# Performance work log

Hardware: AMD Instinct MI355X
Metric: run time of the kernel (lower is better)

The kernel has to match this reference:

```python
import jax, jax.numpy as jnp
import numpy as np
from jax import lax

SIGMA = 1.0
ALPHA = 1.0
BETA = 1.0
TRUNCATE = 4.0  # scipy.ndimage default


def _gauss_kernel(sigma):
    radius = int(TRUNCATE * sigma + 0.5)  # scipy radius rule -> 4 for sigma=1
    x = np.arange(-radius, radius + 1, dtype=np.float64)
    k = np.exp(-0.5 * (x / sigma) ** 2)
    k = (k / k.sum()).astype(np.float32)
    return k

_KERNEL = _gauss_kernel(SIGMA)


def _blur_axis(img, k, axis):
    # scipy mode='reflect' == jnp.pad mode='symmetric' (edge repeated)
    r = len(k) // 2
    pad = [(0, 0)] * img.ndim
    pad[axis] = (r, r)
    xp = jnp.pad(img, pad, mode='symmetric')
    n = img.shape[axis]
    out = k[0] * lax.slice_in_dim(xp, 0, n, axis=axis)
    for i in range(1, len(k)):
        out = out + k[i] * lax.slice_in_dim(xp, i, i + n, axis=axis)
    return out


def gaussian_blur(img):
    # scalar sigma in scipy blurs along EVERY axis, including batch & channel
    k = jnp.asarray(_KERNEL, dtype=img.dtype)
    for ax in range(img.ndim):
        img = _blur_axis(img, k, ax)
    return img


def decompose(I):
    I_log = jnp.log(I + 1e-6)
    I_smooth = gaussian_blur(I_log)
    R = I_log - I_smooth
    L = I_log - R  # == I_smooth
    return jnp.exp(L), jnp.exp(R)


def setup_inputs() -> dict:
    key = jax.random.key(0)
    k1, k2 = jax.random.split(key)
    shape = (16, 3, 512, 512)
    I_enhanced = jax.random.uniform(k1, shape, dtype=jnp.float32)
    I_gt = jax.random.uniform(k2, shape, dtype=jnp.float32)
    return {"I_enhanced": I_enhanced, "I_gt": I_gt}


def reference(I_enhanced, I_gt):
    L_enh, R_enh = decompose(I_enhanced)
    L_gt, R_gt = decompose(I_gt)
    L_reflectance = jnp.mean((R_enh - R_gt) ** 2)
    L_illumination = jnp.mean((L_enh - L_gt) ** 2)
    return ALPHA * L_reflectance + BETA * L_illumination
```

## Files before the change

kernel.cpp:

```cpp
#include <hip/hip_runtime.h>
#include <hip/hip_fp16.h>
#include <cmath>

#define PLANE (512*512)
#define NPLANES 48
#define NEL (48*PLANE)

struct Taps { float k[9]; };
struct CMat { float w[3][3]; };


__global__ __launch_bounds__(64)
void k_blur_hw(const float* __restrict__ inE, const float* __restrict__ inG,
               ushort* __restrict__ ws, Taps tp)
{
    const int l    = threadIdx.x;
    const int w0   = (blockIdx.x & 1) * 256;
    const int r0   = (blockIdx.x >> 1) * 32;
    const int z    = blockIdx.y;

    const float* src = (z < NPLANES) ? (inE + z * PLANE)
                                     : (inG + (z - NPLANES) * PLANE);

    const int  col   = w0 + 4 * l;
    const bool is0   = (l == 0);
    const bool is63  = (l == 63);
    const bool ledge = (w0 == 0);
    const bool redge = (w0 + 256 == 512);
    const bool do_halo = (is0 && !ledge) || (is63 && !redge);
    const int  hoff  = is0 ? (w0 - 4) : (w0 + 256);
    const int  tile  = col >> 6;
    const int  inner = col & 63;

    float ring[10][4];

#define FOLD(r) ((r) < 0 ? (-1 - (r)) : ((r) > 511 ? (1023 - (r)) : (r)))

    float4 pown[3], phal[3];
    phal[0] = phal[1] = phal[2] = make_float4(1.f, 1.f, 1.f, 1.f);
#pragma unroll
    for (int s = 0; s < 3; ++s) {
        const float* rp = src + FOLD(r0 - 4 + s) * 512;
        pown[s] = *(const float4*)(rp + col);
        if (do_halo) phal[s] = *(const float4*)(rp + hoff);
    }

    for (int jb = 0; jb < 40; jb += 10) {
#pragma unroll
        for (int u = 0; u < 10; ++u) {
            const int j = jb + u;

            float4 own = pown[0], hal = phal[0];
            pown[0] = pown[1]; pown[1] = pown[2];
            phal[0] = phal[1]; phal[1] = phal[2];
            if (j + 3 < 40) {
                const float* rp = src + FOLD(r0 - 1 + j) * 512;
                pown[2] = *(const float4*)(rp + col);
                if (do_halo) phal[2] = *(const float4*)(rp + hoff);
            }

            const float w4 = __logf(own.x + 1e-6f);
            const float w5 = __logf(own.y + 1e-6f);
            const float w6 = __logf(own.z + 1e-6f);
            const float w7 = __logf(own.w + 1e-6f);
            const float h0 = __logf(hal.x + 1e-6f);
            const float h1 = __logf(hal.y + 1e-6f);
            const float h2 = __logf(hal.z + 1e-6f);
            const float h3 = __logf(hal.w + 1e-6f);

            float win[12];
            win[4] = w4; win[5] = w5; win[6] = w6; win[7] = w7;
            win[0] = __shfl_up(w4, 1);
            win[1] = __shfl_up(w5, 1);
            win[2] = __shfl_up(w6, 1);
            win[3] = __shfl_up(w7, 1);
            win[8]  = __shfl_down(w4, 1);
            win[9]  = __shfl_down(w5, 1);
            win[10] = __shfl_down(w6, 1);
            win[11] = __shfl_down(w7, 1);
            if (is0) {
                if (ledge) { win[0] = w7; win[1] = w6; win[2] = w5; win[3] = w4; }
                else       { win[0] = h0; win[1] = h1; win[2] = h2; win[3] = h3; }
            }
            if (is63) {
                if (redge) { win[8] = w7; win[9] = w6; win[10] = w5; win[11] = w4; }
                else       { win[8] = h0; win[9] = h1; win[10] = h2; win[11] = h3; }
            }

#pragma unroll
            for (int i = 0; i < 4; ++i) {
                float o = 0.f;
#pragma unroll
                for (int t = 0; t < 9; ++t) o += tp.k[t] * win[i + t];
                ring[u][i] = o;
            }

            if (j >= 8) {
                float acc[4];
#pragma unroll
                for (int i = 0; i < 4; ++i) {
                    float o = 0.f;
#pragma unroll
                    for (int t = 0; t < 9; ++t)
                        o += tp.k[t] * ring[(u + 2 + t) % 10][i];
                    acc[i] = o;
                }
                const int ro = r0 + j - 8;
                __half2 pa, pb;
                pa.x = __float2half(acc[0]); pa.y = __float2half(acc[1]);
                pb.x = __float2half(acc[2]); pb.y = __float2half(acc[3]);
                ushort* dp = ws + (((ro * 8 + tile) * 96) + z) * 64 + inner;
                *(uint2*)dp = make_uint2(*(uint*)&pa, *(uint*)&pb);
            }
        }
    }
#undef FOLD
}

__global__ __launch_bounds__(256)
void k_cn_loss(const ushort* __restrict__ ws, const float* __restrict__ Ie,
               const float* __restrict__ Ig, float* __restrict__ out,
               Taps tp, CMat cm)
{
    const int tid = threadIdx.x;
    const int P   = blockIdx.x * 256 + tid;
    const int hw0 = P * 2;
    const ushort* wbase = ws + (hw0 >> 6) * (96 * 64) + (hw0 & 63);

    __half2 k2[9], cw[3][3];
#pragma unroll
    for (int t = 0; t < 9; ++t) k2[t] = __float2half2_rn(tp.k[t]);
#pragma unroll
    for (int i = 0; i < 3; ++i)
#pragma unroll
        for (int j = 0; j < 3; ++j) cw[i][j] = __float2half2_rn(cm.w[i][j]);

    __half2 re[9][3];
    __half2 rg[9][3];

#define LOADRAW(m, uE, uG)                                                     \
    uE[0] = *(const uint*)(wbase + ((m) * 3 + 0) * 64);                        \
    uE[1] = *(const uint*)(wbase + ((m) * 3 + 1) * 64);                        \
    uE[2] = *(const uint*)(wbase + ((m) * 3 + 2) * 64);                        \
    uG[0] = *(const uint*)(wbase + (48 + (m) * 3 + 0) * 64);                   \
    uG[1] = *(const uint*)(wbase + (48 + (m) * 3 + 1) * 64);                   \
    uG[2] = *(const uint*)(wbase + (48 + (m) * 3 + 2) * 64);

#define CBLUR(u, dst)                                                          \
    {                                                                          \
        __half2 v0 = *(__half2*)&u[0];                                         \
        __half2 v1 = *(__half2*)&u[1];                                         \
        __half2 v2 = *(__half2*)&u[2];                                         \
        dst[0] = __hfma2(cw[0][0], v0, __hfma2(cw[0][1], v1, __hmul2(cw[0][2], v2))); \
        dst[1] = __hfma2(cw[1][0], v0, __hfma2(cw[1][1], v1, __hmul2(cw[1][2], v2))); \
        dst[2] = __hfma2(cw[2][0], v0, __hfma2(cw[2][1], v1, __hmul2(cw[2][2], v2))); \
    }

#pragma unroll
    for (int m = 0; m < 4; ++m) {
        uint uE[3], uG[3];
        LOADRAW(m, uE, uG);
        CBLUR(uE, re[m]); CBLUR(uG, rg[m]);
    }
    uint nuE[3], nuG[3];
    LOADRAW(4, nuE, nuG);
    float2 ieq[3], igq[3];
#pragma unroll
    for (int c = 0; c < 3; ++c) {
        ieq[c] = *(const float2*)(Ie + c * PLANE + hw0);
        igq[c] = *(const float2*)(Ig + c * PLANE + hw0);
    }

    float acc = 0.f;
#pragma unroll
    for (int n = 0; n < 16; ++n) {
        float2 nie[3], nig[3];
        if (n + 1 < 16) {
#pragma unroll
            for (int c = 0; c < 3; ++c) {
                nie[c] = *(const float2*)(Ie + ((n + 1) * 3 + c) * PLANE + hw0);
                nig[c] = *(const float2*)(Ig + ((n + 1) * 3 + c) * PLANE + hw0);
            }
        }
        const int mnew = n + 4;
        if (mnew < 16) {
            CBLUR(nuE, re[mnew % 9]); CBLUR(nuG, rg[mnew % 9]);
            if (mnew + 1 < 16) { LOADRAW(mnew + 1, nuE, nuG); }
        }
#pragma unroll
        for (int c = 0; c < 3; ++c) {
            __half2 se2 = __float2half2_rn(0.f), sg2 = se2;
#pragma unroll
            for (int t = 0; t < 9; ++t) {
                int m = n - 4 + t;
                m = (m < 0) ? (-1 - m) : ((m > 15) ? (31 - m) : m);
                se2 = __hfma2(k2[t], re[m % 9][c], se2);
                sg2 = __hfma2(k2[t], rg[m % 9][c], sg2);
            }
            const float se0 = __half2float(__low2half(se2));
            const float se1 = __half2float(__high2half(se2));
            const float sg0 = __half2float(__low2half(sg2));
            const float sg1 = __half2float(__high2half(sg2));

            {
                float ee = __expf(-se0), eg = __expf(-sg0);
                float Re = (ieq[c].x + 1e-6f) * ee;
                float Rg = (igq[c].x + 1e-6f) * eg;
                float Le = __builtin_amdgcn_rcpf(ee);
                float Lg = __builtin_amdgcn_rcpf(eg);
                float dr = Re - Rg, dl = Le - Lg;
                acc += dr * dr + dl * dl;
            }
            {
                float ee = __expf(-se1), eg = __expf(-sg1);
                float Re = (ieq[c].y + 1e-6f) * ee;
                float Rg = (igq[c].y + 1e-6f) * eg;
                float Le = __builtin_amdgcn_rcpf(ee);
                float Lg = __builtin_amdgcn_rcpf(eg);
                float dr = Re - Rg, dl = Le - Lg;
                acc += dr * dr + dl * dl;
            }
        }
        if (n + 1 < 16) {
#pragma unroll
            for (int c = 0; c < 3; ++c) { ieq[c] = nie[c]; igq[c] = nig[c]; }
        }
    }
#undef LOADRAW
#undef CBLUR

    __shared__ float red[256];
    red[tid] = acc;
    __syncthreads();
#pragma unroll
    for (int s = 128; s > 0; s >>= 1) {
        if (tid < s) red[tid] += red[tid + s];
        __syncthreads();
    }
    if (tid == 0) atomicAdd(out, red[0] * (1.0f / (float)NEL));
}

extern "C" void kernel_launch(void* const* d_in, const int* in_sizes, int n_in,
                              void* d_out, int out_size, void* d_ws, size_t ws_size,
                              hipStream_t stream) {
    const float* Ie = (const float*)d_in[0];
    const float* Ig = (const float*)d_in[1];

    Taps tp;
    {
        double kk[9], s = 0.0;
        for (int i = 0; i < 9; ++i) { double x = (double)(i - 4); kk[i] = exp(-0.5 * x * x); s += kk[i]; }
        for (int i = 0; i < 9; ++i) tp.k[i] = (float)(kk[i] / s);
    }

    CMat cm;
    {
        for (int c = 0; c < 3; ++c) {
            cm.w[c][0] = cm.w[c][1] = cm.w[c][2] = 0.f;
            for (int t = 0; t < 9; ++t) {
                int m = c - 4 + t;
                int mm = ((m % 6) + 6) % 6;
                if (mm > 2) mm = 5 - mm;
                cm.w[c][mm] += tp.k[t];
            }
        }
    }

    ushort* ws = (ushort*)d_ws;

    hipMemsetAsync(d_out, 0, sizeof(float), stream);
    dim3 g1(32, 96);
    k_blur_hw<<<g1, 64, 0, stream>>>(Ie, Ig, ws, tp);
    k_cn_loss<<<512, 256, 0, stream>>>(ws, Ie, Ig, (float*)d_out, tp, cm);
}
```

Before: 173.1 us.

## Stash fp16 input copy in tiled workspace and use half2 vertical blur

The first kernel now also writes an fp16 copy of (I+1e-6) into a second workspace laid out in the same tiled order as the blurred data. The second kernel reads that half-precision copy instead of re-reading the fp32 inputs, which halves those bytes and makes the accesses match the workspace layout. The vertical blur pass now keeps its ring buffer in half2 and accumulates with packed fp16 FMAs. This lowers register use and ALU work, but adds fp16 rounding to the input values and to the intermediate blur, and adds an extra write in the first kernel.

```diff
diff --git a/kernel.cpp b/kernel.cpp
--- a/kernel.cpp
+++ b/kernel.cpp
@@ -12,7 +12,7 @@
 
 __global__ __launch_bounds__(64)
 void k_blur_hw(const float* __restrict__ inE, const float* __restrict__ inG,
-               ushort* __restrict__ ws, Taps tp)
+               ushort* __restrict__ wsS, ushort* __restrict__ wsI, Taps tp)
 {
     const int l    = threadIdx.x;
     const int w0   = (blockIdx.x & 1) * 256;
@@ -32,7 +32,11 @@
     const int  tile  = col >> 6;
     const int  inner = col & 63;
 
-    float ring[10][4];
+    __half2 kh[9];
+#pragma unroll
+    for (int t = 0; t < 9; ++t) kh[t] = __float2half2_rn(tp.k[t]);
+
+    __half2 ring[10][2];
 
 #define FOLD(r) ((r) < 0 ? (-1 - (r)) : ((r) > 511 ? (1023 - (r)) : (r)))
 
@@ -57,6 +61,14 @@
                 const float* rp = src + FOLD(r0 - 1 + j) * 512;
                 pown[2] = *(const float4*)(rp + col);
                 if (do_halo) phal[2] = *(const float4*)(rp + hoff);
+            }
+
+            if (j >= 4 && j < 36) {
+                const int ri = r0 + j - 4;
+                __half2 i0 = __floats2half2_rn(own.x + 1e-6f, own.y + 1e-6f);
+                __half2 i1 = __floats2half2_rn(own.z + 1e-6f, own.w + 1e-6f);
+                ushort* dpI = wsI + (((ri * 8 + tile) * 96) + z) * 64 + inner;
+                *(uint2*)dpI = make_uint2(*(uint*)&i0, *(uint*)&i1);
             }
 
             const float w4 = __logf(own.x + 1e-6f);
@@ -87,30 +99,31 @@
                 else       { win[8] = h0; win[9] = h1; win[10] = h2; win[11] = h3; }
             }
 
-#pragma unroll
-            for (int i = 0; i < 4; ++i) {
-                float o = 0.f;
-#pragma unroll
-                for (int t = 0; t < 9; ++t) o += tp.k[t] * win[i + t];
-                ring[u][i] = o;
+            {
+                float o0 = 0.f, o1 = 0.f, o2 = 0.f, o3 = 0.f;
+#pragma unroll
+                for (int t = 0; t < 9; ++t) {
+                    const float kt = tp.k[t];
+                    o0 += kt * win[t];
+                    o1 += kt * win[t + 1];
+                    o2 += kt * win[t + 2];
+                    o3 += kt * win[t + 3];
+                }
+                ring[u][0] = __floats2half2_rn(o0, o1);
+                ring[u][1] = __floats2half2_rn(o2, o3);
             }
 
             if (j >= 8) {
-                float acc[4];
-#pragma unroll
-                for (int i = 0; i < 4; ++i) {
-                    float o = 0.f;
-#pragma unroll
-                    for (int t = 0; t < 9; ++t)
-                        o += tp.k[t] * ring[(u + 2 + t) % 10][i];
-                    acc[i] = o;
+                __half2 a0 = __float2half2_rn(0.f), a1 = a0;
+#pragma unroll
+                for (int t = 0; t < 9; ++t) {
+                    const int sl = (u + 2 + t) % 10;
+                    a0 = __hfma2(kh[t], ring[sl][0], a0);
+                    a1 = __hfma2(kh[t], ring[sl][1], a1);
                 }
                 const int ro = r0 + j - 8;
-                __half2 pa, pb;
-                pa.x = __float2half(acc[0]); pa.y = __float2half(acc[1]);
-                pb.x = __float2half(acc[2]); pb.y = __float2half(acc[3]);
-                ushort* dp = ws + (((ro * 8 + tile) * 96) + z) * 64 + inner;
-                *(uint2*)dp = make_uint2(*(uint*)&pa, *(uint*)&pb);
+                ushort* dpS = wsS + (((ro * 8 + tile) * 96) + z) * 64 + inner;
+                *(uint2*)dpS = make_uint2(*(uint*)&a0, *(uint*)&a1);
             }
         }
     }
@@ -118,14 +131,15 @@
 }
 
 __global__ __launch_bounds__(256)
-void k_cn_loss(const ushort* __restrict__ ws, const float* __restrict__ Ie,
-               const float* __restrict__ Ig, float* __restrict__ out,
-               Taps tp, CMat cm)
+void k_cn_loss(const ushort* __restrict__ wsS, const ushort* __restrict__ wsI,
+               float* __restrict__ out, Taps tp, CMat cm)
 {
     const int tid = threadIdx.x;
     const int P   = blockIdx.x * 256 + tid;
     const int hw0 = P * 2;
-    const ushort* wbase = ws + (hw0 >> 6) * (96 * 64) + (hw0 & 63);
+    const int off = (hw0 >> 6) * (96 * 64) + (hw0 & 63);
+    const ushort* sbase = wsS + off;
+    const ushort* ibase = wsI + off;
 
     __half2 k2[9], cw[3][3];
 #pragma unroll
@@ -139,12 +153,12 @@
     __half2 rg[9][3];
 
 #define LOADRAW(m, uE, uG)                                                     \
-    uE[0] = *(const uint*)(wbase + ((m) * 3 + 0) * 64);                        \
-    uE[1] = *(const uint*)(wbase + ((m) * 3 + 1) * 64);                        \
-    uE[2] = *(const uint*)(wbase + ((m) * 3 + 2) * 64);                        \
-    uG[0] = *(const uint*)(wbase + (48 + (m) * 3 + 0) * 64);                   \
-    uG[1] = *(const uint*)(wbase + (48 + (m) * 3 + 1) * 64);                   \
-    uG[2] = *(const uint*)(wbase + (48 + (m) * 3 + 2) * 64);
+    uE[0] = *(const uint*)(sbase + ((m) * 3 + 0) * 64);                        \
+    uE[1] = *(const uint*)(sbase + ((m) * 3 + 1) * 64);                        \
+    uE[2] = *(const uint*)(sbase + ((m) * 3 + 2) * 64);                        \
+    uG[0] = *(const uint*)(sbase + (48 + (m) * 3 + 0) * 64);                   \
+    uG[1] = *(const uint*)(sbase + (48 + (m) * 3 + 1) * 64);                   \
+    uG[2] = *(const uint*)(sbase + (48 + (m) * 3 + 2) * 64);
 
 #define CBLUR(u, dst)                                                          \
     {                                                                          \
@@ -164,22 +178,22 @@
     }
     uint nuE[3], nuG[3];
     LOADRAW(4, nuE, nuG);
-    float2 ieq[3], igq[3];
+    uint ieq[3], igq[3];
 #pragma unroll
     for (int c = 0; c < 3; ++c) {
-        ieq[c] = *(const float2*)(Ie + c * PLANE + hw0);
-        igq[c] = *(const float2*)(Ig + c * PLANE + hw0);
+        ieq[c] = *(const uint*)(ibase + c * 64);
+        igq[c] = *(const uint*)(ibase + (48 + c) * 64);
     }
 
     float acc = 0.f;
 #pragma unroll
     for (int n = 0; n < 16; ++n) {
-        float2 nie[3], nig[3];
+        uint nie[3], nig[3];
         if (n + 1 < 16) {
 #pragma unroll
             for (int c = 0; c < 3; ++c) {
-                nie[c] = *(const float2*)(Ie + ((n + 1) * 3 + c) * PLANE + hw0);
-                nig[c] = *(const float2*)(Ig + ((n + 1) * 3 + c) * PLANE + hw0);
+                nie[c] = *(const uint*)(ibase + (((n + 1) * 3 + c)) * 64);
+                nig[c] = *(const uint*)(ibase + ((48 + (n + 1) * 3 + c)) * 64);
             }
         }
         const int mnew = n + 4;
@@ -197,24 +211,24 @@
                 se2 = __hfma2(k2[t], re[m % 9][c], se2);
                 sg2 = __hfma2(k2[t], rg[m % 9][c], sg2);
             }
-            const float se0 = __half2float(__low2half(se2));
-            const float se1 = __half2float(__high2half(se2));
-            const float sg0 = __half2float(__low2half(sg2));
-            const float sg1 = __half2float(__high2half(sg2));
+            const float2 sef = __half22float2(se2);
+            const float2 sgf = __half22float2(sg2);
+            const float2 ief = __half22float2(*(__half2*)&ieq[c]);
+            const float2 igf = __half22float2(*(__half2*)&igq[c]);
 
             {
-                float ee = __expf(-se0), eg = __expf(-sg0);
-                float Re = (ieq[c].x + 1e-6f) * ee;
-                float Rg = (igq[c].x + 1e-6f) * eg;
+                float ee = __expf(-sef.x), eg = __expf(-sgf.x);
+                float Re = ief.x * ee;
+                float Rg = igf.x * eg;
                 float Le = __builtin_amdgcn_rcpf(ee);
                 float Lg = __builtin_amdgcn_rcpf(eg);
                 float dr = Re - Rg, dl = Le - Lg;
                 acc += dr * dr + dl * dl;
             }
             {
-                float ee = __expf(-se1), eg = __expf(-sg1);
-                float Re = (ieq[c].y + 1e-6f) * ee;
-                float Rg = (igq[c].y + 1e-6f) * eg;
+                float ee = __expf(-sef.y), eg = __expf(-sgf.y);
+                float Re = ief.y * ee;
+                float Rg = igf.y * eg;
                 float Le = __builtin_amdgcn_rcpf(ee);
                 float Lg = __builtin_amdgcn_rcpf(eg);
                 float dr = Re - Rg, dl = Le - Lg;
@@ -266,10 +280,11 @@
         }
     }
 
-    ushort* ws = (ushort*)d_ws;
+    ushort* wsS = (ushort*)d_ws;
+    ushort* wsI = wsS + 2 * (size_t)NEL;
 
     hipMemsetAsync(d_out, 0, sizeof(float), stream);
     dim3 g1(32, 96);
-    k_blur_hw<<<g1, 64, 0, stream>>>(Ie, Ig, ws, tp);
-    k_cn_loss<<<512, 256, 0, stream>>>(ws, Ie, Ig, (float*)d_out, tp, cm);
+    k_blur_hw<<<g1, 64, 0, stream>>>(Ie, Ig, wsS, wsI, tp);
+    k_cn_loss<<<512, 256, 0, stream>>>(wsS, wsI, (float*)d_out, tp, cm);
 }
```

Result: faster. 165.1 us (-4.6%).
